# Kernel optimization log

Hardware: AMD Instinct MI355X
Metric: run time of the kernel (lower is better)

Reference implementation:

```python
import jax, jax.numpy as jnp
import numpy as np

D_MODEL = 1024
N_HEADS = 16
D_K = 64

def setup_inputs() -> dict:
    key = jax.random.key(0)
    k0, k1, k2, k3, k4 = jax.random.split(key, 5)
    B, S = 4, 4096
    std = 0.02
    x = jax.random.normal(k0, (B, S, D_MODEL), dtype=jnp.float32)
    # nn.Linear weights are [out, in]; init normal(0, 0.02) as in _init_weights
    W_q = std * jax.random.normal(k1, (N_HEADS * D_K, D_MODEL), dtype=jnp.float32)
    W_k = std * jax.random.normal(k2, (N_HEADS * D_K, D_MODEL), dtype=jnp.float32)
    W_v = std * jax.random.normal(k3, (N_HEADS * D_K, D_MODEL), dtype=jnp.float32)
    W_o = std * jax.random.normal(k4, (D_MODEL, N_HEADS * D_K), dtype=jnp.float32)
    return {"x": x, "W_q": W_q, "W_k": W_k, "W_v": W_v, "W_o": W_o}

def reference(x, W_q, W_k, W_v, W_o):
    B, S, _ = x.shape
    H, Dk = N_HEADS, D_K
    # projections (nn.Linear: x @ W.T), reshape to [B, S, H, Dk]
    q = (x @ W_q.T).reshape(B, S, H, Dk)
    k = (x @ W_k.T).reshape(B, S, H, Dk)
    v = (x @ W_v.T).reshape(B, S, H, Dk)
    scale = 1.0 / jnp.sqrt(jnp.float32(Dk))
    # No softmax between the two matmuls -> reassociate (QK^T)V = Q(K^TV),
    # identical math, O(S*d^2) instead of O(S^2*d).
    kv = jnp.einsum('bshd,bshe->bhde', k, v)          # [B, H, Dk, Dk]
    attn = jnp.einsum('bshd,bhde->bshe', q, kv) * scale  # [B, S, H, Dk]
    out = attn.reshape(B, S, H * Dk) @ W_o.T
    return out
```

## Files before the change

### kernel.cpp

```cpp
#include <hip/hip_runtime.h>
#include <hip/hip_bf16.h>
#include <cstdint>


typedef __bf16 bf16x8 __attribute__((ext_vector_type(8)));
typedef float f32x4 __attribute__((ext_vector_type(4)));
typedef unsigned short ushort_t;

__device__ inline void gld_lds16(const void* g, void* l) {
    __builtin_amdgcn_global_load_lds(
        (const __attribute__((address_space(1))) unsigned int*)g,
        (__attribute__((address_space(3))) unsigned int*)l,
        16, 0, 0);
}

__device__ inline ushort_t f2bf(float f) {
    uint32_t u = __float_as_uint(f);
    uint32_t r = (u + 0x7fffu + ((u >> 16) & 1u)) >> 16;
    return (ushort_t)r;
}
__device__ inline float bf2f(ushort_t u) {
    return __uint_as_float((uint32_t)u << 16);
}

template <typename OutT>
__global__ __launch_bounds__(256, 2)
void gemm_bt(const ushort_t* __restrict__ A, int lda, long strideA,
             const ushort_t* __restrict__ B, int ldb, long strideB,
             OutT* __restrict__ C0, int ldc0, long strideC0, int K)
{
    __shared__ ushort_t lA[128 * 32];
    __shared__ ushort_t lB[128 * 32];

    const int t    = threadIdx.x;
    const int lane = t & 63;
    const int wid  = t >> 6;
    const int z    = blockIdx.z;

    A += (size_t)z * strideA;
    B += (size_t)z * strideB;

    const int m0 = blockIdx.x * 128;
    const int n0 = blockIdx.y * 128;

    const int wm = (wid >> 1) * 64;
    const int wn = (wid & 1) * 64;
    const int mr = lane & 15;
    const int q4 = lane >> 4;

    const int row_a = t >> 2;
    const int seg   = ((t & 3) ^ ((t >> 3) & 3)) * 8;
    const int csw   = (q4 ^ ((mr >> 1) & 3)) * 16;

    f32x4 acc[4][4] = {};

    for (int k0 = 0; k0 < K; k0 += 32) {
        __syncthreads();
        gld_lds16(A + (size_t)(m0 + row_a) * lda + k0 + seg,      (char*)lA + wid * 1024);
        gld_lds16(A + (size_t)(m0 + 64 + row_a) * lda + k0 + seg, (char*)lA + 4096 + wid * 1024);
        gld_lds16(B + (size_t)(n0 + row_a) * ldb + k0 + seg,      (char*)lB + wid * 1024);
        gld_lds16(B + (size_t)(n0 + 64 + row_a) * ldb + k0 + seg, (char*)lB + 4096 + wid * 1024);
        __syncthreads();

        bf16x8 af[4], bf[4];
#pragma unroll
        for (int i = 0; i < 4; ++i)
            af[i] = *(const bf16x8*)((const char*)lA + (wm + i * 16 + mr) * 64 + csw);
#pragma unroll
        for (int j = 0; j < 4; ++j)
            bf[j] = *(const bf16x8*)((const char*)lB + (wn + j * 16 + mr) * 64 + csw);
#pragma unroll
        for (int i = 0; i < 4; ++i)
#pragma unroll
            for (int j = 0; j < 4; ++j)
                acc[i][j] = __builtin_amdgcn_mfma_f32_16x16x32_bf16(af[i], bf[j], acc[i][j], 0, 0, 0);
    }

    OutT* Cw = C0 + (size_t)z * strideC0;
#pragma unroll
    for (int i = 0; i < 4; ++i) {
        const int rbase = m0 + wm + i * 16 + q4 * 4;
#pragma unroll
        for (int j = 0; j < 4; ++j) {
            const int col = n0 + wn + j * 16 + mr;
#pragma unroll
            for (int r = 0; r < 4; ++r) {
                const float v = acc[i][j][r];
                const size_t off = (size_t)(rbase + r) * ldc0 + col;
                if constexpr (sizeof(OutT) == 2) Cw[off] = f2bf(v);
                else                             Cw[off] = v;
            }
        }
    }
}

__global__ __launch_bounds__(512, 2)
void gemm256_bt(const ushort_t* __restrict__ A, int lda, long strideA,
                const ushort_t* __restrict__ B, int ldb, long strideB,
                float* __restrict__ C, int ldc, long strideC, int K)
{
    __shared__ char lds[131072];

    const int t    = threadIdx.x;
    const int lane = t & 63;
    const int wid  = t >> 6;
    const int z    = blockIdx.z;

    A += (size_t)z * strideA;
    B += (size_t)z * strideB;

    const int m0 = blockIdx.x * 256;
    const int n0 = blockIdx.y * 256;

    const int wm = wid >> 2;
    const int wn = wid & 3;
    const int mr = lane & 15;
    const int q4 = lane >> 4;

    const int NT = K >> 6;

    const int srow = t >> 3;
    const int scol = ((t & 7) << 3) ^ (((t >> 3) & 7) << 3);

    auto stage_half = [&](const ushort_t* __restrict__ src, int ld, int org,
                          int h, int tgt, int bsel) {
        if (tgt >= NT) return;
        char* base = lds + bsel + ((tgt & 1) << 15) + (h << 14) + wid * 1024;
        const ushort_t* g = src + (size_t)(org + h * 128 + srow) * ld + tgt * 64 + scol;
        gld_lds16(g, base);
        gld_lds16(g + ((size_t)ld << 6), base + 8192);
    };
    auto stage_unit = [&](int u, int tgt) {
        if (u < 2) stage_half(B, ldb, n0, u,     tgt, 65536);
        else       stage_half(A, lda, m0, u - 2, tgt, 0);
    };

    stage_unit(0, 0); stage_unit(1, 0); stage_unit(2, 0); stage_unit(3, 0);
    stage_unit(0, 1); stage_unit(1, 1); stage_unit(2, 1);
    asm volatile("s_waitcnt vmcnt(6)" ::: "memory");
    __builtin_amdgcn_s_barrier();

    f32x4 acc[8][4] = {};

    for (int kt = 0; kt < NT; ++kt) {
        const char* aBuf = lds + ((kt & 1) << 15) + (wm << 14);
        const char* bBuf = lds + 65536 + ((kt & 1) << 15) + ((wn >> 1) << 14);
        const int cb = (wn & 1) << 6;

        bf16x8 bB[4][2];
#pragma unroll
        for (int p = 0; p < 4; ++p) {
            bf16x8 aA[2][2];
#pragma unroll
            for (int s = 0; s < 2; ++s) {
                const int lr = (2 * p + s) * 16 + mr;
                const int kx = (lr & 7) << 4;
#pragma unroll
                for (int ks = 0; ks < 2; ++ks)
                    aA[s][ks] = *(const bf16x8*)(aBuf + lr * 128 + ((ks * 64 + q4 * 16) ^ kx));
            }
            if (p == 0) {
#pragma unroll
                for (int j = 0; j < 4; ++j) {
                    const int c  = cb + j * 16 + mr;
                    const int kx = (c & 7) << 4;
#pragma unroll
                    for (int ks = 0; ks < 2; ++ks)
                        bB[j][ks] = *(const bf16x8*)(bBuf + c * 128 + ((ks * 64 + q4 * 16) ^ kx));
                }
            }
            if      (p == 0) stage_unit(3, kt + 1);
            else if (p == 1) stage_unit(0, kt + 2);
            else if (p == 2) stage_unit(1, kt + 2);
            else             stage_unit(2, kt + 2);

            __builtin_amdgcn_s_barrier();
            asm volatile("s_waitcnt lgkmcnt(0)" ::: "memory");
            __builtin_amdgcn_sched_barrier(0);

            __builtin_amdgcn_s_setprio(1);
#pragma unroll
            for (int s = 0; s < 2; ++s)
#pragma unroll
                for (int j = 0; j < 4; ++j)
#pragma unroll
                    for (int ks = 0; ks < 2; ++ks)
                        acc[2 * p + s][j] = __builtin_amdgcn_mfma_f32_16x16x32_bf16(
                            aA[s][ks], bB[j][ks], acc[2 * p + s][j], 0, 0, 0);
            __builtin_amdgcn_s_setprio(0);
            __builtin_amdgcn_sched_barrier(0);

            if (p == 3) {
                if (kt == NT - 2)     asm volatile("s_waitcnt vmcnt(0)" ::: "memory");
                else if (kt < NT - 2) asm volatile("s_waitcnt vmcnt(6)" ::: "memory");
            }
            __builtin_amdgcn_s_barrier();
        }
    }

    float* Cw = C + (size_t)z * strideC;
#pragma unroll
    for (int i = 0; i < 8; ++i) {
        const int row = m0 + wm * 128 + i * 16 + q4 * 4;
#pragma unroll
        for (int j = 0; j < 4; ++j) {
            const int col = n0 + wn * 64 + j * 16 + mr;
#pragma unroll
            for (int r = 0; r < 4; ++r)
                Cw[(size_t)(row + r) * ldc + col] = acc[i][j][r];
        }
    }
}

__global__ __launch_bounds__(256, 2)
void gemm_gram(const ushort_t* __restrict__ X, ushort_t* __restrict__ Gp)
{
    __shared__ ushort_t lA[128 * 32];
    __shared__ ushort_t lB[128 * 32];

    const int t    = threadIdx.x;
    const int lane = t & 63;
    const int wid  = t >> 6;

    const int z  = blockIdx.x;
    const int bb = z >> 2, ks = z & 3;

    int ti = 0, rem = blockIdx.y;
    while (rem >= 8 - ti) { rem -= 8 - ti; ++ti; }
    const int tj = ti + rem;
    const int m0 = ti * 128;
    const int n0 = tj * 128;

    const ushort_t* A = X + (size_t)bb * 4096 + (size_t)ks * 1024;

    const int wm = (wid >> 1) * 64;
    const int wn = (wid & 1) * 64;
    const int mr = lane & 15;
    const int q4 = lane >> 4;

    const int row_a = t >> 2;
    const int seg   = ((t & 3) ^ ((t >> 3) & 3)) * 8;
    const int csw   = (q4 ^ ((mr >> 1) & 3)) * 16;

    f32x4 acc[4][4] = {};

    for (int k0 = 0; k0 < 1024; k0 += 32) {
        __syncthreads();
        gld_lds16(A + (size_t)(m0 + row_a) * 16384 + k0 + seg,      (char*)lA + wid * 1024);
        gld_lds16(A + (size_t)(m0 + 64 + row_a) * 16384 + k0 + seg, (char*)lA + 4096 + wid * 1024);
        gld_lds16(A + (size_t)(n0 + row_a) * 16384 + k0 + seg,      (char*)lB + wid * 1024);
        gld_lds16(A + (size_t)(n0 + 64 + row_a) * 16384 + k0 + seg, (char*)lB + 4096 + wid * 1024);
        __syncthreads();

        bf16x8 af[4], bf[4];
#pragma unroll
        for (int i = 0; i < 4; ++i)
            af[i] = *(const bf16x8*)((const char*)lA + (wm + i * 16 + mr) * 64 + csw);
#pragma unroll
        for (int j = 0; j < 4; ++j)
            bf[j] = *(const bf16x8*)((const char*)lB + (wn + j * 16 + mr) * 64 + csw);
#pragma unroll
        for (int i = 0; i < 4; ++i)
#pragma unroll
            for (int j = 0; j < 4; ++j)
                acc[i][j] = __builtin_amdgcn_mfma_f32_16x16x32_bf16(af[i], bf[j], acc[i][j], 0, 0, 0);
    }

    ushort_t* Cw = Gp + ((size_t)z << 20);
#pragma unroll
    for (int i = 0; i < 4; ++i) {
        const int rbase = m0 + wm + i * 16 + q4 * 4;
#pragma unroll
        for (int j = 0; j < 4; ++j) {
            const int col = n0 + wn + j * 16 + mr;
#pragma unroll
            for (int r = 0; r < 4; ++r)
                Cw[(size_t)(rbase + r) * 1024 + col] = f2bf(acc[i][j][r]);
        }
    }
}

__global__ __launch_bounds__(256)
void reduce_g_t(const ushort_t* __restrict__ Gp, ushort_t* __restrict__ G)
{
    __shared__ float acc[64 * 65];

    const int t  = threadIdx.x;
    const int b  = blockIdx.y;
    const int tr = blockIdx.x >> 4, tc = blockIdx.x & 15;
    const int sr = (tr <= tc) ? tr : tc;
    const int sc = (tr <= tc) ? tc : tr;
    const bool flip = tr > tc;

#pragma unroll
    for (int p = 0; p < 4; ++p) {
        const int idx = p * 256 + t;
        const int r = idx >> 4, c = (idx & 15) * 4;
        float a0 = 0.f, a1 = 0.f, a2 = 0.f, a3 = 0.f;
#pragma unroll
        for (int ksl = 0; ksl < 4; ++ksl) {
            const ushort4 u = *(const ushort4*)&Gp[((size_t)(b * 4 + ksl) << 20)
                                                   + (size_t)(sr * 64 + r) * 1024 + sc * 64 + c];
            a0 += bf2f(u.x); a1 += bf2f(u.y); a2 += bf2f(u.z); a3 += bf2f(u.w);
        }
        acc[r * 65 + c + 0] = a0;
        acc[r * 65 + c + 1] = a1;
        acc[r * 65 + c + 2] = a2;
        acc[r * 65 + c + 3] = a3;
    }
    __syncthreads();

#pragma unroll
    for (int p = 0; p < 4; ++p) {
        const int idx = p * 256 + t;
        const int r = idx >> 4, c = (idx & 15) * 4;
        float v0, v1, v2, v3;
        if (flip) {
            v0 = acc[(c + 0) * 65 + r];
            v1 = acc[(c + 1) * 65 + r];
            v2 = acc[(c + 2) * 65 + r];
            v3 = acc[(c + 3) * 65 + r];
        } else {
            v0 = acc[r * 65 + c + 0];
            v1 = acc[r * 65 + c + 1];
            v2 = acc[r * 65 + c + 2];
            v3 = acc[r * 65 + c + 3];
        }
        ushort4 o;
        o.x = f2bf(v0); o.y = f2bf(v1); o.z = f2bf(v2); o.w = f2bf(v3);
        *(ushort4*)&G[((size_t)b << 20) + (size_t)(tr * 64 + r) * 1024 + tc * 64 + c] = o;
    }
}

__global__ __launch_bounds__(256)
void cast_x_t(const float* __restrict__ x, ushort_t* __restrict__ xb,
              ushort_t* __restrict__ xbT)
{
    __shared__ ushort_t lt[64 * 66];
    const int t  = threadIdx.x;
    const int s0 = blockIdx.x * 64;
    const int i0 = blockIdx.y * 64;

#pragma unroll
    for (int c = 0; c < 4; ++c) {
        const int idx = c * 256 + t;
        const int r = idx >> 4, c4 = (idx & 15) * 4;
        const float4 f = *(const float4*)&x[(size_t)(s0 + r) * 1024 + i0 + c4];
        ushort4 o;
        o.x = f2bf(f.x); o.y = f2bf(f.y); o.z = f2bf(f.z); o.w = f2bf(f.w);
        *(ushort4*)&xb[(size_t)(s0 + r) * 1024 + i0 + c4] = o;
        *(uint32_t*)&lt[r * 66 + c4]     = (uint32_t)o.x | ((uint32_t)o.y << 16);
        *(uint32_t*)&lt[r * 66 + c4 + 2] = (uint32_t)o.z | ((uint32_t)o.w << 16);
    }
    __syncthreads();
#pragma unroll
    for (int c = 0; c < 4; ++c) {
        const int idx = c * 256 + t;
        const int ri = idx >> 4, s4 = (idx & 15) * 4;
        ushort4 o;
        o.x = lt[(s4 + 0) * 66 + ri];
        o.y = lt[(s4 + 1) * 66 + ri];
        o.z = lt[(s4 + 2) * 66 + ri];
        o.w = lt[(s4 + 3) * 66 + ri];
        *(ushort4*)&xbT[(size_t)(i0 + ri) * 16384 + s0 + s4] = o;
    }
}

__global__ __launch_bounds__(256)
void cast_wt(const float* __restrict__ W, ushort_t* __restrict__ WT)
{
    __shared__ ushort_t lt[64 * 66];
    const int t  = threadIdx.x;
    const int r0 = blockIdx.x * 64;
    const int c0 = blockIdx.y * 64;

#pragma unroll
    for (int c = 0; c < 4; ++c) {
        const int idx = c * 256 + t;
        const int r = idx >> 4, c4 = (idx & 15) * 4;
        const float4 f = *(const float4*)&W[(size_t)(r0 + r) * 1024 + c0 + c4];
        ushort4 o;
        o.x = f2bf(f.x); o.y = f2bf(f.y); o.z = f2bf(f.z); o.w = f2bf(f.w);
        *(uint32_t*)&lt[r * 66 + c4]     = (uint32_t)o.x | ((uint32_t)o.y << 16);
        *(uint32_t*)&lt[r * 66 + c4 + 2] = (uint32_t)o.z | ((uint32_t)o.w << 16);
    }
    __syncthreads();
#pragma unroll
    for (int c = 0; c < 4; ++c) {
        const int idx = c * 256 + t;
        const int ri = idx >> 4, s4 = (idx & 15) * 4;
        ushort4 o;
        o.x = lt[(s4 + 0) * 66 + ri];
        o.y = lt[(s4 + 1) * 66 + ri];
        o.z = lt[(s4 + 2) * 66 + ri];
        o.w = lt[(s4 + 3) * 66 + ri];
        *(ushort4*)&WT[(size_t)(c0 + ri) * 1024 + r0 + s4] = o;
    }
}

__global__ __launch_bounds__(256)
void cast_w2(const float* __restrict__ a, const float* __restrict__ b,
             ushort_t* __restrict__ out)
{
    const float* src = (blockIdx.y == 0) ? a : b;
    const int i = (blockIdx.x * 256 + threadIdx.x) * 4;
    const float4 f = *(const float4*)&src[i];
    ushort4 o;
    o.x = f2bf(f.x); o.y = f2bf(f.y); o.z = f2bf(f.z); o.w = f2bf(f.w);
    *(ushort4*)&out[(size_t)blockIdx.y * 1048576 + i] = o;
}

__global__ __launch_bounds__(256)
void kvblk(const ushort_t* __restrict__ H, const ushort_t* __restrict__ Wv,
           float* __restrict__ KVp)
{
    __shared__ ushort_t sH[64 * 132];
    __shared__ ushort_t sV[64 * 132];

    const int t  = threadIdx.x;
    const int is = blockIdx.x;
    const int bh = blockIdx.y;
    const int b  = bh >> 4, h = bh & 15;

    const ushort_t* Hp = H + ((size_t)b << 20) + (size_t)(h * 64) * 1024 + is * 128;
    const ushort_t* Vp = Wv + (size_t)(h * 64) * 1024 + is * 128;

#pragma unroll
    for (int i2 = 0; i2 < 8; ++i2) {
        const int ci = i2 * 256 + t;
        const int r = ci >> 5, c = (ci & 31) * 4;
        *(uint2*)&sH[r * 132 + c] = *(const uint2*)&Hp[(size_t)r * 1024 + c];
        *(uint2*)&sV[r * 132 + c] = *(const uint2*)&Vp[(size_t)r * 1024 + c];
    }
    __syncthreads();

    const int d0 = (t >> 4) * 4;
    const int e0 = (t & 15) * 4;
    float acc[4][4] = {};

#pragma unroll 2
    for (int i4 = 0; i4 < 128; i4 += 4) {
        uint2 hu[4], vu[4];
#pragma unroll
        for (int j = 0; j < 4; ++j) {
            hu[j] = *(const uint2*)&sH[(d0 + j) * 132 + i4];
            vu[j] = *(const uint2*)&sV[(e0 + j) * 132 + i4];
        }
        float hf[4][4], vf[4][4];
#pragma unroll
        for (int j = 0; j < 4; ++j) {
            hf[j][0] = __uint_as_float(hu[j].x << 16);
            hf[j][1] = __uint_as_float(hu[j].x & 0xffff0000u);
            hf[j][2] = __uint_as_float(hu[j].y << 16);
            hf[j][3] = __uint_as_float(hu[j].y & 0xffff0000u);
            vf[j][0] = __uint_as_float(vu[j].x << 16);
            vf[j][1] = __uint_as_float(vu[j].x & 0xffff0000u);
            vf[j][2] = __uint_as_float(vu[j].y << 16);
            vf[j][3] = __uint_as_float(vu[j].y & 0xffff0000u);
        }
#pragma unroll
        for (int ii = 0; ii < 4; ++ii)
#pragma unroll
            for (int di = 0; di < 4; ++di)
#pragma unroll
                for (int ej = 0; ej < 4; ++ej)
                    acc[di][ej] += hf[di][ii] * vf[ej][ii];
    }

    float* outp = KVp + ((size_t)(is * 64 + bh)) * 4096;
#pragma unroll
    for (int i = 0; i < 4; ++i) {
        float4 o; o.x = acc[i][0]; o.y = acc[i][1]; o.z = acc[i][2]; o.w = acc[i][3];
        *(float4*)&outp[(d0 + i) * 64 + e0] = o;
    }
}

__global__ __launch_bounds__(256)
void reduce_kv8(const float4* __restrict__ in, float4* __restrict__ out)
{
    const int i = blockIdx.x * 256 + threadIdx.x;
    float4 a = in[i];
#pragma unroll
    for (int s = 1; s < 8; ++s) {
        const float4 b = in[s * 65536 + i];
        a.x += b.x; a.y += b.y; a.z += b.z; a.w += b.w;
    }
    out[i] = a;
}

__global__ __launch_bounds__(256)
void make_E(const float* __restrict__ KV, const float* __restrict__ Wo,
            ushort_t* __restrict__ Et)
{
    __shared__ float skv[64 * 65];
    __shared__ float swo[64 * 65];

    const int t  = threadIdx.x;
    const int bh = blockIdx.y;
    const int b  = bh >> 4, h = bh & 15;
    const int j0 = blockIdx.x * 64;

    const float* kvp = KV + (size_t)bh * 4096;
#pragma unroll
    for (int i = 0; i < 4; ++i) {
        const int idx = t + i * 256;
        const int r = idx >> 4, c = (idx & 15) * 4;
        const float4 f = *(const float4*)&kvp[r * 64 + c];
        skv[r * 65 + c + 0] = f.x;
        skv[r * 65 + c + 1] = f.y;
        skv[r * 65 + c + 2] = f.z;
        skv[r * 65 + c + 3] = f.w;
        const float4 g = *(const float4*)&Wo[(size_t)(j0 + r) * 1024 + h * 64 + c];
        swo[r * 65 + c + 0] = g.x;
        swo[r * 65 + c + 1] = g.y;
        swo[r * 65 + c + 2] = g.z;
        swo[r * 65 + c + 3] = g.w;
    }
    __syncthreads();

    const int d0 = (t & 15) * 4;
#pragma unroll
    for (int pass = 0; pass < 4; ++pass) {
        const int jloc = (t >> 4) + pass * 16;
        float s0 = 0.f, s1 = 0.f, s2 = 0.f, s3 = 0.f;
        const float* wrow = &swo[jloc * 65];
#pragma unroll 8
        for (int e = 0; e < 64; ++e) {
            const float w = wrow[e];
            s0 += skv[(d0 + 0) * 65 + e] * w;
            s1 += skv[(d0 + 1) * 65 + e] * w;
            s2 += skv[(d0 + 2) * 65 + e] * w;
            s3 += skv[(d0 + 3) * 65 + e] * w;
        }
        ushort4 o;
        o.x = f2bf(s0 * 0.125f);
        o.y = f2bf(s1 * 0.125f);
        o.z = f2bf(s2 * 0.125f);
        o.w = f2bf(s3 * 0.125f);
        *(ushort4*)&Et[((size_t)b * 1024 + j0 + jloc) * 1024 + h * 64 + d0] = o;
    }
}


extern "C" void kernel_launch(void* const* d_in, const int* in_sizes, int n_in,
                              void* d_out, int out_size, void* d_ws, size_t ws_size,
                              hipStream_t stream)
{
    const float* x  = (const float*)d_in[0];
    const float* Wq = (const float*)d_in[1];
    const float* Wk = (const float*)d_in[2];
    const float* Wv = (const float*)d_in[3];
    const float* Wo = (const float*)d_in[4];
    float* out = (float*)d_out;

    const int B = 4, S = 4096, D = 1024;
    const long MB1 = 1048576;

    char* ws = (char*)d_ws;
    size_t off = 0;
    auto alloc = [&](size_t bytes) -> void* {
        void* p = ws + off;
        off += (bytes + 255) & ~(size_t)255;
        return p;
    };
    ushort_t* xb   = (ushort_t*)alloc((size_t)B * S * D * 2);
    ushort_t* xbT  = (ushort_t*)alloc((size_t)D * B * S * 2);
    ushort_t* wkv  = (ushort_t*)alloc((size_t)2 * D * D * 2);
    ushort_t* wqT  = (ushort_t*)alloc((size_t)D * D * 2);
    ushort_t* Gb   = (ushort_t*)alloc((size_t)B * D * D * 2);
    float*    kvp  = (float*)alloc((size_t)8 * 64 * 4096 * 4);
    float*    kvr  = (float*)alloc((size_t)64 * 4096 * 4);
    ushort_t* Fb   = (ushort_t*)alloc((size_t)B * D * D * 2);
    char*     R1   = (char*)alloc((size_t)16 * MB1 * 2);
    ushort_t* Gp = (ushort_t*)R1;
    ushort_t* Hb = (ushort_t*)R1;
    ushort_t* Et = (ushort_t*)(R1 + 8 * MB1 * 2);
    ushort_t* wkb = wkv;
    ushort_t* wvb = wkv + MB1;

    cast_x_t<<<dim3(256, 16), dim3(256), 0, stream>>>(x, xb, xbT);
    cast_w2<<<dim3(1024, 2), dim3(256), 0, stream>>>(Wk, Wv, wkv);
    cast_wt<<<dim3(16, 16), dim3(256), 0, stream>>>(Wq, wqT);

    gemm_gram<<<dim3(16, 36), dim3(256), 0, stream>>>(xbT, Gp);
    reduce_g_t<<<dim3(256, 4), dim3(256), 0, stream>>>(Gp, Gb);

    gemm_bt<ushort_t><<<dim3(8, 8, 4), dim3(256), 0, stream>>>(
        wkb, D, 0, Gb, D, MB1, Hb, D, MB1, D);

    kvblk<<<dim3(8, 64), dim3(256), 0, stream>>>(Hb, wvb, kvp);
    reduce_kv8<<<dim3(256), dim3(256), 0, stream>>>((const float4*)kvp, (float4*)kvr);

    make_E<<<dim3(16, 64), dim3(256), 0, stream>>>(kvr, Wo, Et);

    gemm_bt<ushort_t><<<dim3(8, 8, 4), dim3(256), 0, stream>>>(
        Et, D, MB1, wqT, D, 0, Fb, D, (long)D * D, D);

    gemm256_bt<<<dim3(16, 4, 4), dim3(512), 0, stream>>>(
        xb, D, (long)S * D, Fb, D, (long)D * D, out, D, (long)S * D, D);
}
```

Before: 307.8 us.

## Prefetch A fragments across phases, stage epilogue through LDS, shrink small-GEMM N tile

The main 256x256 GEMM now double-buffers its A register fragments, so the LDS reads for the next phase and the next k-tile are issued before the current MFMA block. This is meant to hide LDS latency behind matrix work. Its epilogue now stages the accumulators through LDS so each global write is a coalesced 16-byte row store instead of a scattered scalar store. The two 1024x1024 batched GEMMs switch to a 128x64 tile with higher occupancy bounds, doubling the grid for better CU fill, at the cost of reloading A more often.

```diff
diff --git a/kernel.cpp b/kernel.cpp
--- a/kernel.cpp
+++ b/kernel.cpp
@@ -24,13 +24,13 @@
 }
 
 template <typename OutT>
-__global__ __launch_bounds__(256, 2)
-void gemm_bt(const ushort_t* __restrict__ A, int lda, long strideA,
-             const ushort_t* __restrict__ B, int ldb, long strideB,
-             OutT* __restrict__ C0, int ldc0, long strideC0, int K)
+__global__ __launch_bounds__(256, 4)
+void gemm_bt_n64(const ushort_t* __restrict__ A, int lda, long strideA,
+                 const ushort_t* __restrict__ B, int ldb, long strideB,
+                 OutT* __restrict__ C0, int ldc0, long strideC0, int K)
 {
     __shared__ ushort_t lA[128 * 32];
-    __shared__ ushort_t lB[128 * 32];
+    __shared__ ushort_t lB[64 * 32];
 
     const int t    = threadIdx.x;
     const int lane = t & 63;
@@ -41,10 +41,10 @@
     B += (size_t)z * strideB;
 
     const int m0 = blockIdx.x * 128;
-    const int n0 = blockIdx.y * 128;
+    const int n0 = blockIdx.y * 64;
 
     const int wm = (wid >> 1) * 64;
-    const int wn = (wid & 1) * 64;
+    const int wn = (wid & 1) * 32;
     const int mr = lane & 15;
     const int q4 = lane >> 4;
 
@@ -52,27 +52,26 @@
     const int seg   = ((t & 3) ^ ((t >> 3) & 3)) * 8;
     const int csw   = (q4 ^ ((mr >> 1) & 3)) * 16;
 
-    f32x4 acc[4][4] = {};
+    f32x4 acc[4][2] = {};
 
     for (int k0 = 0; k0 < K; k0 += 32) {
         __syncthreads();
         gld_lds16(A + (size_t)(m0 + row_a) * lda + k0 + seg,      (char*)lA + wid * 1024);
         gld_lds16(A + (size_t)(m0 + 64 + row_a) * lda + k0 + seg, (char*)lA + 4096 + wid * 1024);
         gld_lds16(B + (size_t)(n0 + row_a) * ldb + k0 + seg,      (char*)lB + wid * 1024);
-        gld_lds16(B + (size_t)(n0 + 64 + row_a) * ldb + k0 + seg, (char*)lB + 4096 + wid * 1024);
         __syncthreads();
 
-        bf16x8 af[4], bf[4];
+        bf16x8 af[4], bf[2];
 #pragma unroll
         for (int i = 0; i < 4; ++i)
             af[i] = *(const bf16x8*)((const char*)lA + (wm + i * 16 + mr) * 64 + csw);
 #pragma unroll
-        for (int j = 0; j < 4; ++j)
+        for (int j = 0; j < 2; ++j)
             bf[j] = *(const bf16x8*)((const char*)lB + (wn + j * 16 + mr) * 64 + csw);
 #pragma unroll
         for (int i = 0; i < 4; ++i)
 #pragma unroll
-            for (int j = 0; j < 4; ++j)
+            for (int j = 0; j < 2; ++j)
                 acc[i][j] = __builtin_amdgcn_mfma_f32_16x16x32_bf16(af[i], bf[j], acc[i][j], 0, 0, 0);
     }
 
@@ -81,7 +80,7 @@
     for (int i = 0; i < 4; ++i) {
         const int rbase = m0 + wm + i * 16 + q4 * 4;
 #pragma unroll
-        for (int j = 0; j < 4; ++j) {
+        for (int j = 0; j < 2; ++j) {
             const int col = n0 + wn + j * 16 + mr;
 #pragma unroll
             for (int r = 0; r < 4; ++r) {
@@ -116,6 +115,7 @@
     const int wn = wid & 3;
     const int mr = lane & 15;
     const int q4 = lane >> 4;
+    const int cb = (wn & 1) << 6;
 
     const int NT = K >> 6;
 
@@ -135,79 +135,120 @@
         else       stage_half(A, lda, m0, u - 2, tgt, 0);
     };
 
+    bf16x8 aX[2][2], aY[2][2], bB[4][2];
+
+    auto rdA = [&](bf16x8 (&dst)[2][2], const char* aBuf, int p) {
+#pragma unroll
+        for (int s = 0; s < 2; ++s) {
+            const int lr = (2 * p + s) * 16 + mr;
+            const int kx = (lr & 7) << 4;
+#pragma unroll
+            for (int ks = 0; ks < 2; ++ks)
+                dst[s][ks] = *(const bf16x8*)(aBuf + lr * 128 + ((ks * 64 + q4 * 16) ^ kx));
+        }
+    };
+    auto rdB = [&](const char* bBuf) {
+#pragma unroll
+        for (int j = 0; j < 4; ++j) {
+            const int c  = cb + j * 16 + mr;
+            const int kx = (c & 7) << 4;
+#pragma unroll
+            for (int ks = 0; ks < 2; ++ks)
+                bB[j][ks] = *(const bf16x8*)(bBuf + c * 128 + ((ks * 64 + q4 * 16) ^ kx));
+        }
+    };
+
+    f32x4 acc[8][4] = {};
+    auto MM = [&](int p, bf16x8 (&a)[2][2]) {
+        __builtin_amdgcn_s_setprio(1);
+#pragma unroll
+        for (int s = 0; s < 2; ++s)
+#pragma unroll
+            for (int j = 0; j < 4; ++j)
+#pragma unroll
+                for (int ks = 0; ks < 2; ++ks)
+                    acc[2 * p + s][j] = __builtin_amdgcn_mfma_f32_16x16x32_bf16(
+                        a[s][ks], bB[j][ks], acc[2 * p + s][j], 0, 0, 0);
+        __builtin_amdgcn_s_setprio(0);
+    };
+
+#define BAR()  __builtin_amdgcn_s_barrier()
+#define SB()   __builtin_amdgcn_sched_barrier(0)
+#define LGKM0() asm volatile("s_waitcnt lgkmcnt(0)" ::: "memory")
+
     stage_unit(0, 0); stage_unit(1, 0); stage_unit(2, 0); stage_unit(3, 0);
     stage_unit(0, 1); stage_unit(1, 1); stage_unit(2, 1);
     asm volatile("s_waitcnt vmcnt(6)" ::: "memory");
-    __builtin_amdgcn_s_barrier();
-
-    f32x4 acc[8][4] = {};
+    BAR();
+
+    {
+        const char* a0 = lds + (wm << 14);
+        const char* b0 = lds + 65536 + ((wn >> 1) << 14);
+        rdA(aX, a0, 0);
+        rdB(b0);
+        SB();
+    }
 
     for (int kt = 0; kt < NT; ++kt) {
-        const char* aBuf = lds + ((kt & 1) << 15) + (wm << 14);
-        const char* bBuf = lds + 65536 + ((kt & 1) << 15) + ((wn >> 1) << 14);
-        const int cb = (wn & 1) << 6;
-
-        bf16x8 bB[4][2];
-#pragma unroll
-        for (int p = 0; p < 4; ++p) {
-            bf16x8 aA[2][2];
-#pragma unroll
-            for (int s = 0; s < 2; ++s) {
-                const int lr = (2 * p + s) * 16 + mr;
-                const int kx = (lr & 7) << 4;
-#pragma unroll
-                for (int ks = 0; ks < 2; ++ks)
-                    aA[s][ks] = *(const bf16x8*)(aBuf + lr * 128 + ((ks * 64 + q4 * 16) ^ kx));
+        const char* aBuf  = lds + ((kt & 1) << 15) + (wm << 14);
+        const char* aBufN = lds + (((kt + 1) & 1) << 15) + (wm << 14);
+        const char* bBufN = lds + 65536 + (((kt + 1) & 1) << 15) + ((wn >> 1) << 14);
+
+        stage_unit(3, kt + 1);
+        BAR(); LGKM0(); SB();
+        rdA(aY, aBuf, 1); SB();
+        MM(0, aX); SB();
+        BAR();
+        stage_unit(0, kt + 2);
+        BAR(); LGKM0(); SB();
+        rdA(aX, aBuf, 2); SB();
+        MM(1, aY); SB();
+        BAR();
+        stage_unit(1, kt + 2);
+        BAR(); LGKM0(); SB();
+        rdA(aY, aBuf, 3); SB();
+        MM(2, aX); SB();
+        BAR();
+        stage_unit(2, kt + 2);
+        BAR(); LGKM0(); SB();
+        MM(3, aY); SB();
+        if (kt == NT - 2)     asm volatile("s_waitcnt vmcnt(0)" ::: "memory");
+        else if (kt < NT - 2) asm volatile("s_waitcnt vmcnt(6)" ::: "memory");
+        if (kt + 1 < NT) {
+            rdA(aX, aBufN, 0);
+            rdB(bBufN);
+            SB();
+        }
+        BAR();
+    }
+
+#undef BAR
+#undef SB
+#undef LGKM0
+
+    float* Cw = C + (size_t)z * strideC;
+    float* sf = (float*)lds;
+#pragma unroll
+    for (int h = 0; h < 2; ++h) {
+        if (h) __syncthreads();
+#pragma unroll
+        for (int i2 = 0; i2 < 4; ++i2) {
+            const int rl = wm * 64 + i2 * 16 + q4 * 4;
+#pragma unroll
+            for (int j = 0; j < 4; ++j) {
+                const int cl = wn * 64 + j * 16 + mr;
+#pragma unroll
+                for (int r = 0; r < 4; ++r)
+                    sf[(rl + r) * 256 + cl] = acc[h * 4 + i2][j][r];
             }
-            if (p == 0) {
-#pragma unroll
-                for (int j = 0; j < 4; ++j) {
-                    const int c  = cb + j * 16 + mr;
-                    const int kx = (c & 7) << 4;
-#pragma unroll
-                    for (int ks = 0; ks < 2; ++ks)
-                        bB[j][ks] = *(const bf16x8*)(bBuf + c * 128 + ((ks * 64 + q4 * 16) ^ kx));
-                }
-            }
-            if      (p == 0) stage_unit(3, kt + 1);
-            else if (p == 1) stage_unit(0, kt + 2);
-            else if (p == 2) stage_unit(1, kt + 2);
-            else             stage_unit(2, kt + 2);
-
-            __builtin_amdgcn_s_barrier();
-            asm volatile("s_waitcnt lgkmcnt(0)" ::: "memory");
-            __builtin_amdgcn_sched_barrier(0);
-
-            __builtin_amdgcn_s_setprio(1);
-#pragma unroll
-            for (int s = 0; s < 2; ++s)
-#pragma unroll
-                for (int j = 0; j < 4; ++j)
-#pragma unroll
-                    for (int ks = 0; ks < 2; ++ks)
-                        acc[2 * p + s][j] = __builtin_amdgcn_mfma_f32_16x16x32_bf16(
-                            aA[s][ks], bB[j][ks], acc[2 * p + s][j], 0, 0, 0);
-            __builtin_amdgcn_s_setprio(0);
-            __builtin_amdgcn_sched_barrier(0);
-
-            if (p == 3) {
-                if (kt == NT - 2)     asm volatile("s_waitcnt vmcnt(0)" ::: "memory");
-                else if (kt < NT - 2) asm volatile("s_waitcnt vmcnt(6)" ::: "memory");
-            }
-            __builtin_amdgcn_s_barrier();
-        }
-    }
-
-    float* Cw = C + (size_t)z * strideC;
-#pragma unroll
-    for (int i = 0; i < 8; ++i) {
-        const int row = m0 + wm * 128 + i * 16 + q4 * 4;
-#pragma unroll
-        for (int j = 0; j < 4; ++j) {
-            const int col = n0 + wn * 64 + j * 16 + mr;
-#pragma unroll
-            for (int r = 0; r < 4; ++r)
-                Cw[(size_t)(row + r) * ldc + col] = acc[i][j][r];
+        }
+        __syncthreads();
+#pragma unroll
+        for (int k = 0; k < 16; ++k) {
+            const int rl   = k * 8 + wid;
+            const int grow = m0 + (rl >> 6) * 128 + h * 64 + (rl & 63);
+            const f32x4 v  = *(const f32x4*)&sf[rl * 256 + lane * 4];
+            *(f32x4*)&Cw[(size_t)grow * ldc + n0 + lane * 4] = v;
         }
     }
 }
@@ -585,7 +626,7 @@
     gemm_gram<<<dim3(16, 36), dim3(256), 0, stream>>>(xbT, Gp);
     reduce_g_t<<<dim3(256, 4), dim3(256), 0, stream>>>(Gp, Gb);
 
-    gemm_bt<ushort_t><<<dim3(8, 8, 4), dim3(256), 0, stream>>>(
+    gemm_bt_n64<ushort_t><<<dim3(8, 16, 4), dim3(256), 0, stream>>>(
         wkb, D, 0, Gb, D, MB1, Hb, D, MB1, D);
 
     kvblk<<<dim3(8, 64), dim3(256), 0, stream>>>(Hb, wvb, kvp);
@@ -593,7 +634,7 @@
 
     make_E<<<dim3(16, 64), dim3(256), 0, stream>>>(kvr, Wo, Et);
 
-    gemm_bt<ushort_t><<<dim3(8, 8, 4), dim3(256), 0, stream>>>(
+    gemm_bt_n64<ushort_t><<<dim3(8, 16, 4), dim3(256), 0, stream>>>(
         Et, D, MB1, wqT, D, 0, Fb, D, (long)D * D, D);
 
     gemm256_bt<<<dim3(16, 4, 4), dim3(512), 0, stream>>>(
```

After: 302.9 us. About the same (-1.6%).
